# Kernel tuning notes

Hardware: AMD Instinct MI355X
Metric: run time of the kernel (lower is better)

Reference implementation:

```python
import jax, jax.numpy as jnp
import numpy as np

N_IN = 4096
N_REC = 4096
DT = 1.0
DECAY_V = 0.9            # hard-coded self._decay_v in the source
ETA1 = 0.00157
ETA2 = 0.05749
THETA = 0.2206
FILT = 50.0              # activity_filt_coeff
A0_CONST = 2.0 * N_REC / N_IN


def setup_inputs() -> dict:
    key = jax.random.key(0)
    k1, k2, k3 = jax.random.split(key, 3)
    inputs = jax.random.normal(k1, (1, N_IN), dtype=jnp.float32)
    w_in = jax.random.normal(k2, (N_IN, N_REC), dtype=jnp.float32) / np.sqrt(N_IN).astype(np.float32)
    thresholds = jax.random.uniform(k3, (1, N_REC), dtype=jnp.float32)  # rd.uniform(0,1) in source
    v = jnp.zeros((1, N_REC), dtype=jnp.float32)
    i_state = jnp.zeros((1, N_REC), dtype=jnp.float32)
    z = jnp.zeros((1, N_REC), dtype=jnp.float32)
    A = jnp.zeros((1, 1), dtype=jnp.float32)
    return {"inputs": inputs, "v": v, "i_state": i_state, "z": z, "A": A,
            "w_in": w_in, "thresholds": thresholds}


def reference(inputs, v, i_state, z, A, w_in, thresholds):
    f32 = jnp.float32
    # synaptic input current: [1, n_rec]
    inp_spike_current = inputs @ w_in
    # lif_dynamics2: new_v = v + (1 - decay_v) * (-v + I)
    new_v = v + (1.0 - DECAY_V) * (-v + inp_spike_current)
    # stochastic spike: tanh(v) > uniform threshold
    spk = (jnp.tanh(new_v) > thresholds).astype(f32)
    # reset (multiplying by all-ones mask when no spikes is identical to the tf.cond branch)
    new_v = new_v * (1.0 - spk)
    new_i = new_v  # lif_dynamics2 returns (new_v, new_v, new_z)
    new_z = spk * (1.0 / DT)
    # filtered population activity, A: [1, 1], reduce_sum is global
    pop_activity = A + (1.0 / FILT) * (jnp.sum(new_z) - A)
    x = pop_activity / A0_CONST
    tan = jnp.tanh(x) * (x > 0.0).astype(f32)          # fi_filter
    surprise = ETA1 * tan + ETA2 * tan * (x > THETA).astype(f32)  # [1, 1]
    # mask zeros first half of the input neurons
    mask = jnp.concatenate([jnp.zeros((1, N_IN // 2), f32), jnp.ones((1, N_IN // 2), f32)], axis=1)
    masked_input = inputs * mask
    # outer-product weight delta: [n_in, n_rec]
    dw_ik = -jnp.einsum('bi,bk->ki', inp_spike_current, masked_input) * surprise
    # sign-constraint clip masks (Dale-like constraints on lower half of inputs)
    clip_max = jnp.full((N_IN, N_REC), jnp.inf, f32).at[N_IN // 2:, :N_REC // 2].set(0.0)
    clip_min = jnp.full((N_IN, N_REC), -jnp.inf, f32).at[N_IN // 2:, N_REC // 2:].set(0.0)
    new_w_in = jnp.clip(w_in + dw_ik, clip_min, clip_max)
    # track_vars=False path returns (new_z, state); we also surface the updated w_in
    return (new_z, new_v, new_i, pop_activity, new_w_in)
```

## Files before the change

### kernel.cpp

```cpp
#include <hip/hip_runtime.h>
#include <math.h>

constexpr int N_IN  = 4096;
constexpr int N_REC = 4096;
constexpr int NCHUNK = 64;
constexpr int ROWS   = N_IN / NCHUNK;

__global__ __launch_bounds__(256) void k1_gemv_partial(
    const float* __restrict__ x, const float* __restrict__ w,
    float* __restrict__ partials)
{
    const int chunk = blockIdx.y;
    const int c0 = (blockIdx.x * 256 + threadIdx.x) * 4;

    __shared__ float xs[ROWS];
    if (threadIdx.x < ROWS) xs[threadIdx.x] = x[chunk * ROWS + threadIdx.x];
    __syncthreads();

    const float* wp = w + (size_t)chunk * ROWS * N_REC + c0;
    float4 acc = {0.f, 0.f, 0.f, 0.f};
#pragma unroll 8
    for (int r = 0; r < ROWS; ++r) {
        float4 wv = *(const float4*)(wp + (size_t)r * N_REC);
        const float xr = xs[r];
        acc.x = fmaf(xr, wv.x, acc.x);
        acc.y = fmaf(xr, wv.y, acc.y);
        acc.z = fmaf(xr, wv.z, acc.z);
        acc.w = fmaf(xr, wv.w, acc.w);
    }
    *(float4*)(partials + (size_t)chunk * N_REC + c0) = acc;
}

__global__ __launch_bounds__(256) void k2_lif(
    const float* __restrict__ partials, const float* __restrict__ v_in,
    const float* __restrict__ thr, float* __restrict__ out,
    float* __restrict__ isc, float* __restrict__ blockSums)
{
    const int col = blockIdx.x * 256 + threadIdx.x;

    float I = 0.f;
#pragma unroll 8
    for (int p = 0; p < NCHUNK; ++p) I += partials[(size_t)p * N_REC + col];
    isc[col] = I;

    const float v  = v_in[col];
    float nv = v + 0.1f * (I - v);
    const float spk = (tanhf(nv) > thr[col]) ? 1.0f : 0.0f;
    nv = nv * (1.0f - spk);

    out[col]             = spk;
    out[N_REC + col]     = nv;
    out[2 * N_REC + col] = nv;

    float s = spk;
#pragma unroll
    for (int o = 32; o > 0; o >>= 1) s += __shfl_down(s, o, 64);
    __shared__ float wsum[4];
    const int lane = threadIdx.x & 63, wid = threadIdx.x >> 6;
    if (lane == 0) wsum[wid] = s;
    __syncthreads();
    if (threadIdx.x == 0)
        blockSums[blockIdx.x] = wsum[0] + wsum[1] + wsum[2] + wsum[3];
}

__global__ void k3_scalar(
    const float* __restrict__ blockSums, const float* __restrict__ A,
    float* __restrict__ out_pop, float* __restrict__ surprise)
{
    if (threadIdx.x == 0) {
        float s = 0.f;
#pragma unroll
        for (int i = 0; i < 16; ++i) s += blockSums[i];
        const float a   = A[0];
        const float pop = a + (1.0f / 50.0f) * (s - a);
        out_pop[0] = pop;
        const float x = pop * 0.5f;
        const float t = (x > 0.0f) ? tanhf(x) : 0.0f;
        float sur = 0.00157f * t;
        if (x > 0.2206f) sur += 0.05749f * t;
        surprise[0] = sur;
    }
}

__global__ __launch_bounds__(256) void k4_wupdate(
    const float* __restrict__ w, const float* __restrict__ x,
    const float* __restrict__ isc, const float* __restrict__ surprise,
    float* __restrict__ wout)
{
    const unsigned gid = blockIdx.x * 256 + threadIdx.x;
    const int k  = gid >> 10;
    const int i0 = (gid & 1023) << 2;
    const size_t off = (size_t)k * N_REC + i0;

    float4 wv = *(const float4*)(w + off);
    float4 o;
    if (k < N_IN / 2) {
        o = wv;
    } else {
        const float coef = -surprise[0] * x[k];
        float4 iv = *(const float4*)(isc + i0);
        o.x = fmaf(coef, iv.x, wv.x);
        o.y = fmaf(coef, iv.y, wv.y);
        o.z = fmaf(coef, iv.z, wv.z);
        o.w = fmaf(coef, iv.w, wv.w);
        if (i0 < N_REC / 2) {
            o.x = fminf(o.x, 0.f); o.y = fminf(o.y, 0.f);
            o.z = fminf(o.z, 0.f); o.w = fminf(o.w, 0.f);
        } else {
            o.x = fmaxf(o.x, 0.f); o.y = fmaxf(o.y, 0.f);
            o.z = fmaxf(o.z, 0.f); o.w = fmaxf(o.w, 0.f);
        }
    }
    float* wo = wout + off;
    wo[0] = o.x; wo[1] = o.y; wo[2] = o.z; wo[3] = o.w;
}

extern "C" void kernel_launch(void* const* d_in, const int* in_sizes, int n_in,
                              void* d_out, int out_size, void* d_ws, size_t ws_size,
                              hipStream_t stream)
{
    const float* inputs = (const float*)d_in[0];
    const float* v      = (const float*)d_in[1];
    const float* A      = (const float*)d_in[4];
    const float* w_in   = (const float*)d_in[5];
    const float* thr    = (const float*)d_in[6];
    float* out = (float*)d_out;

    float* partials  = (float*)d_ws;
    float* isc       = partials + (size_t)NCHUNK * N_REC;
    float* blockSums = isc + N_REC;
    float* surprise  = blockSums + 16;

    k1_gemv_partial<<<dim3(4, NCHUNK), 256, 0, stream>>>(inputs, w_in, partials);
    k2_lif<<<16, 256, 0, stream>>>(partials, v, thr, out, isc, blockSums);
    k3_scalar<<<1, 64, 0, stream>>>(blockSums, A, out + 3 * N_REC, surprise);
    k4_wupdate<<<(N_IN * N_REC / 4) / 256, 256, 0, stream>>>(
        w_in, inputs, isc, surprise, out + 3 * N_REC + 1);
}
```

Measured before the change: 142.8 us.

## Shrink GEMV row chunks and fold scalar surprise kernel into weight update

Reduces rows per GEMV chunk so the partial-sum kernel launches four times as many blocks, raising parallelism on the large weight read. The scalar population/surprise kernel is removed and its computation is redundantly recomputed by every thread of the weight-update kernel, saving a launch and a global round-trip. The tradeoff is a fourfold larger partials buffer that the 16-block LIF kernel must sum serially, adding memory traffic and latency there.

```diff
diff --git a/kernel.cpp b/kernel.cpp
--- a/kernel.cpp
+++ b/kernel.cpp
@@ -3,8 +3,8 @@
 
 constexpr int N_IN  = 4096;
 constexpr int N_REC = 4096;
-constexpr int NCHUNK = 64;
-constexpr int ROWS   = N_IN / NCHUNK;
+constexpr int ROWS   = 16;
+constexpr int NCHUNK = N_IN / ROWS;
 
 __global__ __launch_bounds__(256) void k1_gemv_partial(
     const float* __restrict__ x, const float* __restrict__ w,
@@ -19,7 +19,7 @@
 
     const float* wp = w + (size_t)chunk * ROWS * N_REC + c0;
     float4 acc = {0.f, 0.f, 0.f, 0.f};
-#pragma unroll 8
+#pragma unroll
     for (int r = 0; r < ROWS; ++r) {
         float4 wv = *(const float4*)(wp + (size_t)r * N_REC);
         const float xr = xs[r];
@@ -39,7 +39,7 @@
     const int col = blockIdx.x * 256 + threadIdx.x;
 
     float I = 0.f;
-#pragma unroll 8
+#pragma unroll 16
     for (int p = 0; p < NCHUNK; ++p) I += partials[(size_t)p * N_REC + col];
     isc[col] = I;
 
@@ -63,30 +63,24 @@
         blockSums[blockIdx.x] = wsum[0] + wsum[1] + wsum[2] + wsum[3];
 }
 
-__global__ void k3_scalar(
-    const float* __restrict__ blockSums, const float* __restrict__ A,
-    float* __restrict__ out_pop, float* __restrict__ surprise)
-{
-    if (threadIdx.x == 0) {
-        float s = 0.f;
-#pragma unroll
-        for (int i = 0; i < 16; ++i) s += blockSums[i];
-        const float a   = A[0];
-        const float pop = a + (1.0f / 50.0f) * (s - a);
-        out_pop[0] = pop;
-        const float x = pop * 0.5f;
-        const float t = (x > 0.0f) ? tanhf(x) : 0.0f;
-        float sur = 0.00157f * t;
-        if (x > 0.2206f) sur += 0.05749f * t;
-        surprise[0] = sur;
-    }
-}
-
 __global__ __launch_bounds__(256) void k4_wupdate(
     const float* __restrict__ w, const float* __restrict__ x,
-    const float* __restrict__ isc, const float* __restrict__ surprise,
-    float* __restrict__ wout)
+    const float* __restrict__ isc, const float* __restrict__ blockSums,
+    const float* __restrict__ A, float* __restrict__ wout,
+    float* __restrict__ out_pop)
 {
+    float s = 0.f;
+#pragma unroll
+    for (int i = 0; i < 16; ++i) s += blockSums[i];
+    const float a   = A[0];
+    const float pop = a + (1.0f / 50.0f) * (s - a);
+    const float xp  = pop * 0.5f;
+    const float t   = (xp > 0.0f) ? tanhf(xp) : 0.0f;
+    float sur = 0.00157f * t;
+    if (xp > 0.2206f) sur += 0.05749f * t;
+
+    if (blockIdx.x == 0 && threadIdx.x == 0) out_pop[0] = pop;
+
     const unsigned gid = blockIdx.x * 256 + threadIdx.x;
     const int k  = gid >> 10;
     const int i0 = (gid & 1023) << 2;
@@ -97,7 +91,7 @@
     if (k < N_IN / 2) {
         o = wv;
     } else {
-        const float coef = -surprise[0] * x[k];
+        const float coef = -sur * x[k];
         float4 iv = *(const float4*)(isc + i0);
         o.x = fmaf(coef, iv.x, wv.x);
         o.y = fmaf(coef, iv.y, wv.y);
@@ -129,11 +123,9 @@
     float* partials  = (float*)d_ws;
     float* isc       = partials + (size_t)NCHUNK * N_REC;
     float* blockSums = isc + N_REC;
-    float* surprise  = blockSums + 16;
 
     k1_gemv_partial<<<dim3(4, NCHUNK), 256, 0, stream>>>(inputs, w_in, partials);
     k2_lif<<<16, 256, 0, stream>>>(partials, v, thr, out, isc, blockSums);
-    k3_scalar<<<1, 64, 0, stream>>>(blockSums, A, out + 3 * N_REC, surprise);
     k4_wupdate<<<(N_IN * N_REC / 4) / 256, 256, 0, stream>>>(
-        w_in, inputs, isc, surprise, out + 3 * N_REC + 1);
+        w_in, inputs, isc, blockSums, A, out + 3 * N_REC + 1, out + 3 * N_REC);
 }
```

New measurement: 146.3 us. 2.4% more time.

## Copy unchanged top half via memcpy and realign bottom-half stores to float4

Applied to the files above, without the earlier changes.

The top half of the weight matrix is never modified, so it is now copied with a device-to-device memcpy instead of going through the update kernel. The update kernel now covers only the bottom half. Because the output pointer sits one float past an aligned address, each thread shifts its results by one element using lane shuffles, so every store is an aligned float4 write instead of four scalar stores. Wave-edge lanes recompute their neighbour's values, and the first and last elements get special handling, which adds branch and index complexity. The memcpy also runs as its own operation in the stream.

```diff
diff --git a/kernel.cpp b/kernel.cpp
--- a/kernel.cpp
+++ b/kernel.cpp
@@ -3,8 +3,9 @@
 
 constexpr int N_IN  = 4096;
 constexpr int N_REC = 4096;
-constexpr int NCHUNK = 64;
-constexpr int ROWS   = N_IN / NCHUNK;
+constexpr int ROWS   = 64;
+constexpr int NCHUNK = N_IN / ROWS;
+constexpr unsigned HALF = (unsigned)(N_IN / 2) * N_REC;
 
 __global__ __launch_bounds__(256) void k1_gemv_partial(
     const float* __restrict__ x, const float* __restrict__ w,
@@ -82,37 +83,66 @@
     }
 }
 
-__global__ __launch_bounds__(256) void k4_wupdate(
+__global__ __launch_bounds__(256) void k4_bottom(
     const float* __restrict__ w, const float* __restrict__ x,
     const float* __restrict__ isc, const float* __restrict__ surprise,
-    float* __restrict__ wout)
+    float* __restrict__ wout_b)
 {
-    const unsigned gid = blockIdx.x * 256 + threadIdx.x;
-    const int k  = gid >> 10;
-    const int i0 = (gid & 1023) << 2;
-    const size_t off = (size_t)k * N_REC + i0;
+    const unsigned t    = blockIdx.x * 256 + threadIdx.x;
+    const unsigned LAST = HALF / 4 - 1;
+    const float sur = surprise[0];
 
-    float4 wv = *(const float4*)(w + off);
+    const unsigned base = t << 2;
+    const int k  = (N_IN / 2) + (int)(base >> 12);
+    const int i0 = (int)(base & 4095);
+
+    float4 wv = *(const float4*)(w + (size_t)HALF + base);
+    float4 iv = *(const float4*)(isc + i0);
+    const float coef = -sur * x[k];
     float4 o;
-    if (k < N_IN / 2) {
-        o = wv;
+    o.x = fmaf(coef, iv.x, wv.x);
+    o.y = fmaf(coef, iv.y, wv.y);
+    o.z = fmaf(coef, iv.z, wv.z);
+    o.w = fmaf(coef, iv.w, wv.w);
+    if (i0 < N_REC / 2) {
+        o.x = fminf(o.x, 0.f); o.y = fminf(o.y, 0.f);
+        o.z = fminf(o.z, 0.f); o.w = fminf(o.w, 0.f);
     } else {
-        const float coef = -surprise[0] * x[k];
-        float4 iv = *(const float4*)(isc + i0);
-        o.x = fmaf(coef, iv.x, wv.x);
-        o.y = fmaf(coef, iv.y, wv.y);
-        o.z = fmaf(coef, iv.z, wv.z);
-        o.w = fmaf(coef, iv.w, wv.w);
-        if (i0 < N_REC / 2) {
-            o.x = fminf(o.x, 0.f); o.y = fminf(o.y, 0.f);
-            o.z = fminf(o.z, 0.f); o.w = fminf(o.w, 0.f);
-        } else {
-            o.x = fmaxf(o.x, 0.f); o.y = fmaxf(o.y, 0.f);
-            o.z = fmaxf(o.z, 0.f); o.w = fmaxf(o.w, 0.f);
-        }
+        o.x = fmaxf(o.x, 0.f); o.y = fmaxf(o.y, 0.f);
+        o.z = fmaxf(o.z, 0.f); o.w = fmaxf(o.w, 0.f);
     }
-    float* wo = wout + off;
-    wo[0] = o.x; wo[1] = o.y; wo[2] = o.z; wo[3] = o.w;
+
+    float nx = __shfl_down(o.x, 1);
+    float ny = __shfl_down(o.y, 1);
+    float nz = __shfl_down(o.z, 1);
+
+    const int lane = threadIdx.x & 63;
+    if (lane == 63 && t != LAST) {
+        const unsigned b2 = base + 4;
+        const int k2  = (N_IN / 2) + (int)(b2 >> 12);
+        const int i2  = (int)(b2 & 4095);
+        float4 wv2 = *(const float4*)(w + (size_t)HALF + b2);
+        float4 iv2 = *(const float4*)(isc + i2);
+        const float c2 = -sur * x[k2];
+        nx = fmaf(c2, iv2.x, wv2.x);
+        ny = fmaf(c2, iv2.y, wv2.y);
+        nz = fmaf(c2, iv2.z, wv2.z);
+        if (i2 < N_REC / 2) { nx = fminf(nx, 0.f); ny = fminf(ny, 0.f); nz = fminf(nz, 0.f); }
+        else                { nx = fmaxf(nx, 0.f); ny = fmaxf(ny, 0.f); nz = fmaxf(nz, 0.f); }
+    }
+
+    if (t != LAST) {
+        float4 st = {o.w, nx, ny, nz};
+        *(float4*)(wout_b + base + 3) = st;
+    } else {
+        const float c0 = -sur * x[N_IN / 2];
+        wout_b[0] = fminf(fmaf(c0, isc[0], w[HALF + 0]), 0.f);
+        wout_b[1] = fminf(fmaf(c0, isc[1], w[HALF + 1]), 0.f);
+        wout_b[2] = fminf(fmaf(c0, isc[2], w[HALF + 2]), 0.f);
+        const float ct = -sur * x[N_IN - 1];
+        wout_b[HALF - 1] =
+            fmaxf(fmaf(ct, isc[N_REC - 1], w[2 * HALF - 1]), 0.f);
+    }
 }
 
 extern "C" void kernel_launch(void* const* d_in, const int* in_sizes, int n_in,
@@ -130,10 +160,14 @@
     float* isc       = partials + (size_t)NCHUNK * N_REC;
     float* blockSums = isc + N_REC;
     float* surprise  = blockSums + 16;
+    float* wout      = out + 3 * N_REC + 1;
+
+    hipMemcpyAsync(wout, w_in, (size_t)HALF * sizeof(float),
+                   hipMemcpyDeviceToDevice, stream);
 
     k1_gemv_partial<<<dim3(4, NCHUNK), 256, 0, stream>>>(inputs, w_in, partials);
     k2_lif<<<16, 256, 0, stream>>>(partials, v, thr, out, isc, blockSums);
     k3_scalar<<<1, 64, 0, stream>>>(blockSums, A, out + 3 * N_REC, surprise);
-    k4_wupdate<<<(N_IN * N_REC / 4) / 256, 256, 0, stream>>>(
-        w_in, inputs, isc, surprise, out + 3 * N_REC + 1);
+    k4_bottom<<<(HALF / 4) / 256, 256, 0, stream>>>(
+        w_in, inputs, isc, surprise, wout + HALF);
 }
```

After: 154.4 us. 1.08x slower.
